# Kernel optimization log

Hardware: AMD Instinct MI355X
Metric: run time of the kernel (lower is better)

The kernel has to match this reference:

```python
import jax, jax.numpy as jnp
import numpy as np

B, T, I, H = 64, 512, 512, 512


def setup_inputs() -> dict:
    key = jax.random.key(0)
    ks = jax.random.split(key, 7)
    scale_i = 1.0 / np.sqrt(I)
    scale_h = 1.0 / np.sqrt(H)
    x = jax.random.normal(ks[0], (B, T, I), dtype=jnp.float32)
    h0 = jax.random.normal(ks[1], (B, H), dtype=jnp.float32)
    W_ih = jax.random.normal(ks[2], (3 * H, I), dtype=jnp.float32) * scale_i
    W_hh = jax.random.normal(ks[3], (3 * H, H), dtype=jnp.float32) * scale_h
    b_ih = jax.random.normal(ks[4], (3 * H,), dtype=jnp.float32) * scale_h
    b_hh = jax.random.normal(ks[5], (3 * H,), dtype=jnp.float32) * scale_h
    # ragged lengths, sorted descending (module's slicing logic assumes this)
    lengths = jnp.sort(jax.random.randint(ks[6], (B,), 1, T + 1))[::-1].astype(jnp.int64)
    return {"x": x, "h0": h0, "W_ih": W_ih, "W_hh": W_hh,
            "b_ih": b_ih, "b_hh": b_hh, "lengths": lengths}


def _gru_scan(x, h0, W_ih, W_hh, b_ih, b_hh, lengths):
    # Precompute input projections for all timesteps: [B, T, 3H]
    gi = jnp.einsum('bti,gi->btg', x, W_ih) + b_ih
    lengths = lengths.astype(jnp.int32)

    def step(h, inp):
        gi_t, t = inp  # gi_t: [B, 3H]
        gh = h @ W_hh.T + b_hh  # [B, 3H]
        i_r, i_z, i_n = jnp.split(gi_t, 3, axis=-1)
        h_r, h_z, h_n = jnp.split(gh, 3, axis=-1)
        r = jax.nn.sigmoid(i_r + h_r)
        z = jax.nn.sigmoid(i_z + h_z)
        n = jnp.tanh(i_n + r * h_n)
        h_new = (1.0 - z) * n + z * h
        m = (t < lengths)[:, None]  # ragged mask: valid rows this step
        h_keep = jnp.where(m, h_new, h)        # past-length rows keep last state
        y = jnp.where(m, h_new, 0.0)           # output stays zero past length
        return h_keep, y

    ts = jnp.arange(x.shape[1], dtype=jnp.int32)
    h_final, ys = jax.lax.scan(step, h0, (gi.transpose(1, 0, 2), ts))
    output = ys.transpose(1, 0, 2)  # [B, T, H]
    return output, h_final


def reference(x, h0, W_ih, W_hh, b_ih, b_hh, lengths):
    output, h_final = _gru_scan(x, h0, W_ih, W_hh, b_ih, b_hh, lengths)
    final_state = (h_final[None],)  # (1, B, H), matching unsqueeze(0)
    return output, final_state
```

## Files before the change

### kernel.cpp

```cpp
#include <hip/hip_runtime.h>
#include <stdint.h>

#define Bsz 64
#define Tsz 512
#define HD  512
#define GROUPS 4
#define MEMBERS 16
#define BROWS 16
#define JCH 32
#define NWG (GROUPS*MEMBERS)
#define NTHR 512
#define LROW 520
#define LROWD 260
#define HSLOT (Bsz*HD/2)

typedef __attribute__((ext_vector_type(8))) short bf16x8;
typedef __attribute__((ext_vector_type(4))) float f32x4;
typedef __attribute__((ext_vector_type(4))) uint32_t u32x4;
typedef __attribute__((ext_vector_type(2))) uint32_t u32x2;

#define BAR() asm volatile("s_waitcnt lgkmcnt(0)\n\ts_barrier" ::: "memory")

__device__ __forceinline__ uint32_t f2bf(float f) {
  uint32_t u = __builtin_bit_cast(uint32_t, f);
  return (u + 0x7FFFu + ((u >> 16) & 1u)) >> 16;
}

__device__ __forceinline__ bf16x8 ldwf(const float* __restrict__ W, int row, int k0) {
  const f32x4 a = *reinterpret_cast<const f32x4*>(W + (size_t)row * HD + k0);
  const f32x4 b = *reinterpret_cast<const f32x4*>(W + (size_t)row * HD + k0 + 4);
  bf16x8 r;
  r[0] = (short)f2bf(a.x); r[1] = (short)f2bf(a.y);
  r[2] = (short)f2bf(a.z); r[3] = (short)f2bf(a.w);
  r[4] = (short)f2bf(b.x); r[5] = (short)f2bf(b.y);
  r[6] = (short)f2bf(b.z); r[7] = (short)f2bf(b.w);
  return r;
}

__device__ __forceinline__ void stage_x0(const float* __restrict__ x, int b0,
                                         uint32_t* xl, int tid) {
#pragma unroll
  for (int i = 0; i < 4; ++i) {
    const int fl = tid + i * 512;
    const int row = fl >> 7;
    const int c4 = fl & 127;
    const f32x4 v = *reinterpret_cast<const f32x4*>(
        x + (size_t)(b0 + row) * Tsz * HD + c4 * 4);
    u32x2 w;
    w.x = f2bf(v.x) | (f2bf(v.y) << 16);
    w.y = f2bf(v.z) | (f2bf(v.w) << 16);
    *reinterpret_cast<u32x2*>(xl + row * LROWD + c4 * 2) = w;
  }
}

__global__ void gru_init(const float* __restrict__ h0, uint64_t* __restrict__ hbx) {
  const int i = blockIdx.x * 256 + threadIdx.x;
  if (i < HSLOT) {
    const float a = h0[2 * i], b = h0[2 * i + 1];
    hbx[HSLOT + i] = (uint64_t)(f2bf(a) | (f2bf(b) << 16));
    hbx[i] = 0xFFFFFFFF00000000ull;
  }
}

__global__ void __launch_bounds__(NTHR) gru_persist(
    const float* __restrict__ x, const float* __restrict__ h0,
    const float* __restrict__ Wih, const float* __restrict__ Whh,
    const float* __restrict__ bih, const float* __restrict__ bhh,
    const int* __restrict__ lens,
    float* __restrict__ out, float* __restrict__ outh,
    uint64_t* __restrict__ hbx) {
  __shared__ alignas(16) unsigned short x_lds[2][BROWS * LROW];
  __shared__ alignas(16) unsigned short h_lds[BROWS * LROW];
  __shared__ alignas(16) float s_lds[BROWS][4][JCH];

  const int tid = threadIdx.x;
  const int lane = tid & 63;
  const int wv = tid >> 6;
  const int gid = blockIdx.x & 3;
  const int mem = blockIdx.x >> 2;
  const int b0 = gid * BROWS;
  const int j0 = mem * JCH;

  const int grow = tid >> 5;
  const int gj = tid & 31;
  const float br = bih[j0 + gj] + bhh[j0 + gj];
  const float bz = bih[512 + j0 + gj] + bhh[512 + j0 + gj];
  const float bi_n = bih[1024 + j0 + gj];
  const float bh_n = bhh[1024 + j0 + gj];
  float hprev = h0[(size_t)(b0 + grow) * HD + j0 + gj];
  const int lenr = lens[b0 + grow];
  float* const outp = out + (size_t)(b0 + grow) * Tsz * HD + j0 + gj;

  const int prow = tid >> 5;
  const int pcu = (tid & 31) * 8;
  const uint64_t* psrc = hbx + (size_t)(b0 + prow) * 256 + pcu;

  const int xc4 = tid & 127;
  const int xr0 = tid >> 7;
  const float* xbp[4];
#pragma unroll
  for (int i = 0; i < 4; ++i)
    xbp[i] = x + (size_t)(b0 + xr0 + 4 * i) * Tsz * HD + xc4 * 4;

  const int c = lane & 15;
  const int kg = lane >> 4;
  bf16x8 wfa[16], wfb[16];
  if (wv < 4) {
    const int wrow = (wv >> 1) * 512 + j0 + (wv & 1) * 16 + c;
#pragma unroll
    for (int ks = 0; ks < 16; ++ks) {
      const int k0 = ks * 32 + kg * 8;
      wfa[ks] = ldwf(Wih, wrow, k0);
      wfb[ks] = ldwf(Whh, wrow, k0);
    }
  } else if (wv < 6) {
    const int wrow = 1024 + j0 + (wv - 4) * 16 + c;
#pragma unroll
    for (int ks = 0; ks < 16; ++ks) wfa[ks] = ldwf(Wih, wrow, ks * 32 + kg * 8);
  } else {
    const int wrow = 1024 + j0 + (wv - 6) * 16 + c;
#pragma unroll
    for (int ks = 0; ks < 16; ++ks) wfb[ks] = ldwf(Whh, wrow, ks * 32 + kg * 8);
  }

  stage_x0(x, b0, (uint32_t*)&x_lds[0][0], tid);

  f32x4 xr[4];
#pragma unroll
  for (int i = 0; i < 4; ++i)
    xr[i] = *reinterpret_cast<const f32x4*>(xbp[i] + (size_t)1 * HD);

  float o_pend = 0.f;

  __syncthreads();

  for (int t = 0; t < Tsz; ++t) {
    f32x4 acc0 = {0.f, 0.f, 0.f, 0.f}, acc1 = {0.f, 0.f, 0.f, 0.f};
    {
      const unsigned short* xl = &x_lds[t & 1][0];
      if (wv < 6) {
#pragma unroll
        for (int ks = 0; ks < 16; ks += 2) {
          bf16x8 a0 = *reinterpret_cast<const bf16x8*>(xl + c * LROW + ks * 32 + kg * 8);
          bf16x8 a1 = *reinterpret_cast<const bf16x8*>(xl + c * LROW + (ks + 1) * 32 + kg * 8);
          acc0 = __builtin_amdgcn_mfma_f32_16x16x32_bf16(a0, wfa[ks], acc0, 0, 0, 0);
          acc1 = __builtin_amdgcn_mfma_f32_16x16x32_bf16(a1, wfa[ks + 1], acc1, 0, 0, 0);
        }
      }
    }

    if (t + 1 < Tsz) {
      uint32_t* xl = (uint32_t*)&x_lds[(t + 1) & 1][0];
#pragma unroll
      for (int i = 0; i < 4; ++i) {
        u32x2 w;
        w.x = f2bf(xr[i].x) | (f2bf(xr[i].y) << 16);
        w.y = f2bf(xr[i].z) | (f2bf(xr[i].w) << 16);
        *reinterpret_cast<u32x2*>(xl + (xr0 + 4 * i) * LROWD + xc4 * 2) = w;
      }
    }

    {
      const uint64_t* src = psrc + (size_t)((t + 1) & 1) * HSLOT;
      const uint32_t want = (uint32_t)t;
      uint64_t v[8];
      uint64_t s0;
      do {
        s0 = __hip_atomic_load(src, __ATOMIC_RELAXED, __HIP_MEMORY_SCOPE_AGENT);
      } while ((uint32_t)(s0 >> 32) != want);
      v[0] = s0;
      for (;;) {
        bool ok = true;
#pragma unroll
        for (int i = 1; i < 8; ++i)
          v[i] = __hip_atomic_load(src + i, __ATOMIC_RELAXED, __HIP_MEMORY_SCOPE_AGENT);
#pragma unroll
        for (int i = 1; i < 8; ++i) ok &= ((uint32_t)(v[i] >> 32) == want);
        if (ok) break;
      }
      uint32_t* dst = (uint32_t*)&h_lds[0] + prow * LROWD + pcu;
      u32x4 w0 = {(uint32_t)v[0], (uint32_t)v[1], (uint32_t)v[2], (uint32_t)v[3]};
      u32x4 w1 = {(uint32_t)v[4], (uint32_t)v[5], (uint32_t)v[6], (uint32_t)v[7]};
      *reinterpret_cast<u32x4*>(dst) = w0;
      *reinterpret_cast<u32x4*>(dst + 4) = w1;
    }

    if (t > 0) outp[(size_t)(t - 1) * HD] = o_pend;

    BAR();

    if (t + 2 < Tsz) {
#pragma unroll
      for (int i = 0; i < 4; ++i)
        xr[i] = *reinterpret_cast<const f32x4*>(xbp[i] + (size_t)(t + 2) * HD);
    }

    {
      const unsigned short* hl = &h_lds[0];
      if (wv < 4 || wv >= 6) {
#pragma unroll
        for (int ks = 0; ks < 16; ks += 2) {
          bf16x8 a0 = *reinterpret_cast<const bf16x8*>(hl + c * LROW + ks * 32 + kg * 8);
          bf16x8 a1 = *reinterpret_cast<const bf16x8*>(hl + c * LROW + (ks + 1) * 32 + kg * 8);
          acc0 = __builtin_amdgcn_mfma_f32_16x16x32_bf16(a0, wfb[ks], acc0, 0, 0, 0);
          acc1 = __builtin_amdgcn_mfma_f32_16x16x32_bf16(a1, wfb[ks + 1], acc1, 0, 0, 0);
        }
      }
      const f32x4 acc = acc0 + acc1;
      const int slot = (wv < 4) ? (wv >> 1) : ((wv < 6) ? 2 : 3);
      const int col = (wv & 1) * 16 + c;
#pragma unroll
      for (int q = 0; q < 4; ++q) s_lds[kg * 4 + q][slot][col] = acc[q];
    }
    BAR();

    {
      const float sr = s_lds[grow][0][gj] + br;
      const float sz = s_lds[grow][1][gj] + bz;
      const float si = s_lds[grow][2][gj] + bi_n;
      const float sh = s_lds[grow][3][gj] + bh_n;
      const float r = 1.f / (1.f + __expf(-sr));
      const float z = 1.f / (1.f + __expf(-sz));
      const float n = tanhf(si + r * sh);
      const float hnew = (1.f - z) * n + z * hprev;
      const bool m = (t < lenr);
      const float hk = m ? hnew : hprev;
      const uint32_t ub = f2bf(hk);
      const uint32_t ot = __shfl_xor(ub, 1);
      if ((t + 1 < Tsz) && ((lane & 1) == 0)) {
        const uint32_t word = ub | (ot << 16);
        const uint64_t pkt = ((uint64_t)(uint32_t)(t + 1) << 32) | (uint64_t)word;
        __hip_atomic_store(hbx + (size_t)(t & 1) * HSLOT + (size_t)(b0 + grow) * 256 +
                               ((j0 + gj) >> 1),
                           pkt, __ATOMIC_RELAXED, __HIP_MEMORY_SCOPE_AGENT);
      }
      o_pend = m ? hnew : 0.f;
      hprev = hk;
    }
  }

  outp[(size_t)(Tsz - 1) * HD] = o_pend;
  outh[(size_t)(b0 + grow) * HD + j0 + gj] = hprev;
}

extern "C" void kernel_launch(void* const* d_in, const int* in_sizes, int n_in,
                              void* d_out, int out_size, void* d_ws, size_t ws_size,
                              hipStream_t stream) {
  const float* x = (const float*)d_in[0];
  const float* h0 = (const float*)d_in[1];
  const float* Wih = (const float*)d_in[2];
  const float* Whh = (const float*)d_in[3];
  const float* bih = (const float*)d_in[4];
  const float* bhh = (const float*)d_in[5];
  const int* lens = (const int*)d_in[6];
  float* out = (float*)d_out;
  float* outh = out + (size_t)Bsz * Tsz * HD;

  uint64_t* hbx = (uint64_t*)d_ws;

  gru_init<<<64, 256, 0, stream>>>(h0, hbx);
  gru_persist<<<NWG, NTHR, 0, stream>>>(x, h0, Wih, Whh, bih, bhh, lens,
                                        out, outh, hbx);
}
```

Baseline: 1.413 ms.

## Add per-group arrival flags and vectorized polling of hidden-state exchange

Adds a per-group flag array that each workgroup writes after publishing its slice of the hidden state. Consumers first spin on 16 flags with four wide cache-bypassing loads, then read the tagged h packets with dwordx4 loads and recheck the tags. This replaces the per-thread spin on scalar 64-bit atomic loads, aiming to cut polling latency and memory traffic in the cross-workgroup step barrier. The cost is an extra flag round trip per timestep, and the flag store is relaxed with no ordering guarantee relative to the data stores, which is why the data tags are still checked.

```diff
diff --git a/kernel.cpp b/kernel.cpp
--- a/kernel.cpp
+++ b/kernel.cpp
@@ -53,8 +53,10 @@
   }
 }
 
-__global__ void gru_init(const float* __restrict__ h0, uint64_t* __restrict__ hbx) {
+__global__ void gru_init(const float* __restrict__ h0, uint32_t* __restrict__ flg,
+                         uint64_t* __restrict__ hbx) {
   const int i = blockIdx.x * 256 + threadIdx.x;
+  if (i < 2 * GROUPS * 16) flg[i] = (i < GROUPS * 16) ? 0xFFFFFFFFu : 0u;
   if (i < HSLOT) {
     const float a = h0[2 * i], b = h0[2 * i + 1];
     hbx[HSLOT + i] = (uint64_t)(f2bf(a) | (f2bf(b) << 16));
@@ -68,7 +70,7 @@
     const float* __restrict__ bih, const float* __restrict__ bhh,
     const int* __restrict__ lens,
     float* __restrict__ out, float* __restrict__ outh,
-    uint64_t* __restrict__ hbx) {
+    uint32_t* __restrict__ flg, uint64_t* __restrict__ hbx) {
   __shared__ alignas(16) unsigned short x_lds[2][BROWS * LROW];
   __shared__ alignas(16) unsigned short h_lds[BROWS * LROW];
   __shared__ alignas(16) float s_lds[BROWS][4][JCH];
@@ -91,9 +93,8 @@
   const int lenr = lens[b0 + grow];
   float* const outp = out + (size_t)(b0 + grow) * Tsz * HD + j0 + gj;
 
-  const int prow = tid >> 5;
-  const int pcu = (tid & 31) * 8;
-  const uint64_t* psrc = hbx + (size_t)(b0 + prow) * 256 + pcu;
+  const int q = tid & 127;
+  const int r0 = tid >> 7;
 
   const int xc4 = tid & 127;
   const int xr0 = tid >> 7;
@@ -160,29 +161,61 @@
       }
     }
 
-    {
-      const uint64_t* src = psrc + (size_t)((t + 1) & 1) * HSLOT;
-      const uint32_t want = (uint32_t)t;
-      uint64_t v[8];
-      uint64_t s0;
-      do {
-        s0 = __hip_atomic_load(src, __ATOMIC_RELAXED, __HIP_MEMORY_SCOPE_AGENT);
-      } while ((uint32_t)(s0 >> 32) != want);
-      v[0] = s0;
+    const uint32_t want = (uint32_t)t;
+
+    {
+      const uint32_t* fl = flg + ((((t + 1) & 1) * GROUPS + gid) << 4);
       for (;;) {
+        u32x4 f0, f1, f2, f3;
+        asm volatile(
+            "global_load_dwordx4 %0, %4, off sc0 sc1\n\t"
+            "global_load_dwordx4 %1, %4, off offset:16 sc0 sc1\n\t"
+            "global_load_dwordx4 %2, %4, off offset:32 sc0 sc1\n\t"
+            "global_load_dwordx4 %3, %4, off offset:48 sc0 sc1\n\t"
+            "s_waitcnt vmcnt(0)"
+            : "=&v"(f0), "=&v"(f1), "=&v"(f2), "=&v"(f3)
+            : "v"(fl)
+            : "memory");
         bool ok = true;
 #pragma unroll
-        for (int i = 1; i < 8; ++i)
-          v[i] = __hip_atomic_load(src + i, __ATOMIC_RELAXED, __HIP_MEMORY_SCOPE_AGENT);
-#pragma unroll
-        for (int i = 1; i < 8; ++i) ok &= ((uint32_t)(v[i] >> 32) == want);
+        for (int i = 0; i < 4; ++i)
+          ok &= (f0[i] == want) & (f1[i] == want) & (f2[i] == want) & (f3[i] == want);
         if (ok) break;
       }
-      uint32_t* dst = (uint32_t*)&h_lds[0] + prow * LROWD + pcu;
-      u32x4 w0 = {(uint32_t)v[0], (uint32_t)v[1], (uint32_t)v[2], (uint32_t)v[3]};
-      u32x4 w1 = {(uint32_t)v[4], (uint32_t)v[5], (uint32_t)v[6], (uint32_t)v[7]};
-      *reinterpret_cast<u32x4*>(dst) = w0;
-      *reinterpret_cast<u32x4*>(dst + 4) = w1;
+    }
+
+    {
+      const uint64_t* bp = hbx + (size_t)((t + 1) & 1) * HSLOT;
+      const uint64_t* a0 = bp + (size_t)(b0 + r0) * 256 + q * 2;
+      const uint64_t* a1 = a0 + 4 * 256;
+      const uint64_t* a2 = a0 + 8 * 256;
+      const uint64_t* a3 = a0 + 12 * 256;
+      u32x4 d0, d1, d2, d3;
+      for (;;) {
+        asm volatile(
+            "global_load_dwordx4 %0, %4, off sc0 sc1\n\t"
+            "global_load_dwordx4 %1, %5, off sc0 sc1\n\t"
+            "global_load_dwordx4 %2, %6, off sc0 sc1\n\t"
+            "global_load_dwordx4 %3, %7, off sc0 sc1\n\t"
+            "s_waitcnt vmcnt(0)"
+            : "=&v"(d0), "=&v"(d1), "=&v"(d2), "=&v"(d3)
+            : "v"(a0), "v"(a1), "v"(a2), "v"(a3)
+            : "memory");
+        const bool ok = (d0[1] == want) & (d0[3] == want) & (d1[1] == want) &
+                        (d1[3] == want) & (d2[1] == want) & (d2[3] == want) &
+                        (d3[1] == want) & (d3[3] == want);
+        if (ok) break;
+      }
+      uint32_t* hd = (uint32_t*)&h_lds[0] + q * 2;
+      u32x2 w;
+      w.x = d0[0]; w.y = d0[2];
+      *reinterpret_cast<u32x2*>(hd + (r0) * LROWD) = w;
+      w.x = d1[0]; w.y = d1[2];
+      *reinterpret_cast<u32x2*>(hd + (r0 + 4) * LROWD) = w;
+      w.x = d2[0]; w.y = d2[2];
+      *reinterpret_cast<u32x2*>(hd + (r0 + 8) * LROWD) = w;
+      w.x = d3[0]; w.y = d3[2];
+      *reinterpret_cast<u32x2*>(hd + (r0 + 12) * LROWD) = w;
     }
 
     if (t > 0) outp[(size_t)(t - 1) * HD] = o_pend;
@@ -210,7 +243,7 @@
       const int slot = (wv < 4) ? (wv >> 1) : ((wv < 6) ? 2 : 3);
       const int col = (wv & 1) * 16 + c;
 #pragma unroll
-      for (int q = 0; q < 4; ++q) s_lds[kg * 4 + q][slot][col] = acc[q];
+      for (int qq = 0; qq < 4; ++qq) s_lds[kg * 4 + qq][slot][col] = acc[qq];
     }
     BAR();
 
@@ -234,6 +267,11 @@
                                ((j0 + gj) >> 1),
                            pkt, __ATOMIC_RELAXED, __HIP_MEMORY_SCOPE_AGENT);
       }
+      if ((t + 1 < Tsz) && (tid == 0)) {
+        __hip_atomic_store(flg + (((t & 1) * GROUPS + gid) << 4) + mem,
+                           (uint32_t)(t + 1), __ATOMIC_RELAXED,
+                           __HIP_MEMORY_SCOPE_AGENT);
+      }
       o_pend = m ? hnew : 0.f;
       hprev = hk;
     }
@@ -256,9 +294,10 @@
   float* out = (float*)d_out;
   float* outh = out + (size_t)Bsz * Tsz * HD;
 
-  uint64_t* hbx = (uint64_t*)d_ws;
-
-  gru_init<<<64, 256, 0, stream>>>(h0, hbx);
+  uint32_t* flg = (uint32_t*)d_ws;
+  uint64_t* hbx = (uint64_t*)((char*)d_ws + 512);
+
+  gru_init<<<64, 256, 0, stream>>>(h0, flg, hbx);
   gru_persist<<<NWG, NTHR, 0, stream>>>(x, h0, Wih, Whh, bih, bhh, lens,
-                                        out, outh, hbx);
-}
+                                        out, outh, flg, hbx);
+}
```

Measured after the change: 1.289 ms. 8.7% less time.
